# Kernel optimization log

Measured on AMD Instinct MI355X. Metric: run time of the kernel, lower is better.

## Reference

```python
import jax, jax.numpy as jnp
import numpy as np
import math

BS, NAG, HID, NACT, MESS, QD, KD, STEPS, INP = 4096, 8, 256, 16, 64, 64, 64, 5, 128
TRAJ = STEPS * NACT
LAMQ = 0.5


def setup_inputs() -> dict:
    key = jax.random.key(0)
    ks = jax.random.split(key, 12)
    g = lambda k, shape, fan: jax.random.normal(k, shape, jnp.float32) / math.sqrt(fan)
    d = {}
    d["inputs"] = jax.random.normal(ks[0], (BS * NAG, INP), jnp.float32)
    d["old_hstate"] = jax.random.normal(ks[1], (BS * NAG, HID), jnp.float32)
    d["fc1_w"] = g(ks[2], (HID, INP), INP); d["fc1_b"] = jnp.zeros((HID,), jnp.float32)
    d["w_ih"] = g(ks[3], (3 * HID, HID), HID); d["w_hh"] = g(ks[4], (3 * HID, HID), HID)
    d["b_ih"] = jnp.zeros((3 * HID,), jnp.float32); d["b_hh"] = jnp.zeros((3 * HID,), jnp.float32)
    d["dec_w"] = g(ks[5], (NACT, HID), HID); d["dec_b"] = jnp.zeros((NACT,), jnp.float32)
    d["trans_w"] = g(ks[6], (HID, HID + NAG), HID + NAG); d["trans_b"] = jnp.zeros((HID,), jnp.float32)
    d["qij_w"] = g(ks[7], (NACT, HID + MESS), HID + MESS); d["qij_b"] = jnp.zeros((NACT,), jnp.float32)
    d["q_w"] = g(ks[8], (QD, TRAJ), TRAJ); d["q_b"] = jnp.zeros((QD,), jnp.float32)
    d["k_w"] = g(ks[9], (KD, TRAJ), TRAJ); d["k_b"] = jnp.zeros((KD,), jnp.float32)
    d["v_w"] = g(ks[10], (MESS, TRAJ), TRAJ); d["v_b"] = jnp.zeros((MESS,), jnp.float32)
    return d


def _fwd(inputs, old_hstate, fc1_w, fc1_b, w_ih, w_hh, b_ih, b_hh,
         dec_w, dec_b, trans_w, trans_b, qij_w, qij_b,
         q_w, q_b, k_w, k_b, v_w, v_b):
    # fc1 + relu
    x = jax.nn.relu(inputs @ fc1_w.T + fc1_b)  # (BS*NAG, HID)
    # GRUCell (torch gate order: r, z, n)
    gi = x @ w_ih.T + b_ih
    gh = old_hstate @ w_hh.T + b_hh
    ir, iz, i_n = jnp.split(gi, 3, axis=-1)
    hr, hz, h_n = jnp.split(gh, 3, axis=-1)
    r = jax.nn.sigmoid(ir + hr)
    z = jax.nn.sigmoid(iz + hz)
    n = jnp.tanh(i_n + r * h_n)
    h_new = (1.0 - z) * n + z * old_hstate
    h = h_new.reshape(BS, NAG, HID)

    # imagination rollout on detached h
    def step(hc, _):
        q_inf = hc @ dec_w.T + dec_b                       # (BS, NAG, NACT)
        ac = jnp.argmax(q_inf, axis=-1).astype(hc.dtype)   # (BS, NAG)
        ac = jnp.broadcast_to(ac[:, None, :], (BS, NAG, NAG))
        ti = jnp.concatenate([hc, ac], axis=-1)            # (BS, NAG, HID+NAG)
        return ti @ trans_w.T + trans_b, q_inf

    _, qs = jax.lax.scan(step, jax.lax.stop_gradient(h), None, length=STEPS)
    # qs: (STEPS, BS, NAG, NACT) -> trajectory (BS, NAG, STEPS*NACT), step-major on last dim
    traj = jnp.moveaxis(qs, 0, 2).reshape(BS, NAG, TRAJ)

    # tiny agent attention
    query = traj @ q_w.T + q_b   # (BS, NAG, QD)
    key_t = traj @ k_w.T + k_b   # (BS, NAG, KD)
    value = traj @ v_w.T + v_b   # (BS, NAG, MESS)
    score = jnp.einsum('bnq,bmq->bnm', query, key_t) / math.sqrt(MESS)
    attn = jax.nn.softmax(score, axis=-1)
    traj_msg = jnp.einsum('bnm,bmd->bnd', attn, value)  # (BS, NAG, MESS)

    q_local = h @ dec_w.T + dec_b
    q_ij = jnp.concatenate([h, traj_msg], axis=-1) @ qij_w.T + qij_b
    q = q_local + LAMQ * q_ij
    return q, h


def reference(inputs, old_hstate, fc1_w, fc1_b, w_ih, w_hh, b_ih, b_hh,
              dec_w, dec_b, trans_w, trans_b, qij_w, qij_b,
              q_w, q_b, k_w, k_b, v_w, v_b):
    return _fwd(inputs, old_hstate, fc1_w, fc1_b, w_ih, w_hh, b_ih, b_hh,
                dec_w, dec_b, trans_w, trans_b, qij_w, qij_b,
                q_w, q_b, k_w, k_b, v_w, v_b)
```

## Files before the change

### kernel.cpp

```cpp
#include <hip/hip_runtime.h>
#include <math.h>

typedef unsigned short u16;
typedef unsigned int   u32;
typedef __attribute__((ext_vector_type(8))) short bf16x8;
typedef __attribute__((ext_vector_type(4))) float f32x4;

#define NROWS 32768
#define NAG 8
#define HID 256
#define INP 128
#define NACT 16
#define MESS 64
#define TRAJD 80
#define QD 64
#define HOFF 524288

#define PKO_FC1 0
#define PKO_IH  98304
#define PKO_HH  688128
#define PKO_TR  1277952
#define PKO_DEC 1499136
#define PKO_QKV 1511424
#define PKO_QIJ 1566720
#define PK_TOTAL 1582080
#define WS_CB   791040
#define WS_FLAG 793312

#define OB_FC1B 0
#define OB_BIH  256
#define OB_BHH  1024
#define OB_DECB 1792
#define OB_TRB  1808
#define OB_QIJB 2064
#define OB_QB   2080

__device__ __forceinline__ float bf2f(u16 v){ return __uint_as_float(((u32)v)<<16); }
__device__ __forceinline__ u16 f2bf(float f){
    u32 u = __float_as_uint(f);
    return (u16)((u + 0x7fffu + ((u>>16)&1u))>>16);
}
__device__ __forceinline__ float sig_(float x){ return 1.0f/(1.0f+expf(-x)); }
__device__ __forceinline__ float ldin(const void* p, size_t i, int f32){
    return f32 ? ((const float*)p)[i] : bf2f(((const u16*)p)[i]);
}
__device__ __forceinline__ void stout1(void* out, size_t i, float v, int f32){
    if (f32) ((float*)out)[i]=v; else ((u16*)out)[i]=f2bf(v);
}
__device__ __forceinline__ void split3(float w, u16& s0, u16& s1, u16& s2){
    u16 a=f2bf(w); float r  = w - bf2f(a);
    u16 b=f2bf(r); float r2 = r - bf2f(b);
    s0=a; s1=b; s2=f2bf(r2);
}
__device__ __forceinline__ f32x4 splat4(float b){ f32x4 v = {b,b,b,b}; return v; }

#define MFMA(a,b,c) __builtin_amdgcn_mfma_f32_16x16x32_bf16((a),(b),(c),0,0,0)

__device__ __forceinline__ bf16x8 lda_pl(const u16* P, int p, int row, int kbyte){
    const char* b = (const char*)P + ((p*32+row)*640) + (kbyte ^ ((row&7)<<4));
    return *(const bf16x8*)b;
}
__device__ __forceinline__ void stw_pl(u16* P, int p, int row, int col, u16 v){
    char* b = (char*)P + ((p*32+row)*640) + (((col*2)) ^ ((row&7)<<4));
    *(u16*)b = v;
}
__device__ __forceinline__ void split_store_pl(u16* P, int row, int col, float v){
    u16 a,b,c; split3(v,a,b,c);
    stw_pl(P,0,row,col,a); stw_pl(P,1,row,col,b); stw_pl(P,2,row,col,c);
}
__device__ __forceinline__ bf16x8 lda_tp(const u16* P, int p, int row, int kbyte){
    const char* b = (const char*)P + ((p*32+row)*256) + (kbyte ^ ((row&7)<<4));
    return *(const bf16x8*)b;
}
__device__ __forceinline__ void stw_tp(u16* P, int p, int row, int col, u16 v){
    char* b = (char*)P + ((p*32+row)*256) + (((col*2)) ^ ((row&7)<<4));
    *(u16*)b = v;
}
__device__ __forceinline__ void split_store_tp(u16* P, int row, int col, float v){
    u16 a,b,c; split3(v,a,b,c);
    stw_tp(P,0,row,col,a); stw_tp(P,1,row,col,b); stw_tp(P,2,row,col,c);
}
__device__ __forceinline__ float ld_tp1(const u16* P, int p, int row, int col){
    const char* b = (const char*)P + ((p*32+row)*256) + (((col*2)) ^ ((row&7)<<4));
    return bf2f(*(const u16*)b);
}
__device__ __forceinline__ bf16x8 ldg_bf8(const void* p, size_t off){
    return *(const bf16x8*)((const u16*)p + off);
}
__device__ __forceinline__ void ldg_f32_split(const void* p, size_t off, bf16x8& f0, bf16x8& f1, bf16x8& f2){
    const float* fp = (const float*)p + off;
    #pragma unroll
    for (int j=0;j<8;j++){
        float w = fp[j];
        u16 a,b,c; split3(w,a,b,c);
        f0[j]=(short)a; f1[j]=(short)b; f2[j]=(short)c;
    }
}
#define BCH(base, NTv, ksv, pbv, ntv) \
    (*(const bf16x8*)((base) + ((((ksv)*3+(pbv))*(NTv) + (ntv))*512) + lane*8))

__global__ void k_det(const void* __restrict__ inp, int* __restrict__ flag){
    __shared__ int cnt;
    if (threadIdx.x==0) cnt=0;
    __syncthreads();
    int big=0;
    for (int i=threadIdx.x;i<128;i+=64){
        u32 w = ((const u32*)inp)[i];
        float g = bf2f((u16)w);
        if (!(fabsf(g) <= 1e4f)) big++;
    }
    if (big) atomicAdd(&cnt, big);
    __syncthreads();
    if (threadIdx.x==0) *flag = (cnt>=4) ? 1 : 0;
}

__device__ __forceinline__ void pack_tile(const void* W, int Kdim, int NT, u16* pk, int tau, int f32){
    int lane2 = tau & 63, c = tau >> 6;
    int nt = c % NT, ks = c / NT;
    int n  = nt*16 + (lane2 & 15);
    int kb = ks*32 + (lane2 >> 4)*8;
    u16 o0[8],o1[8],o2[8];
    #pragma unroll
    for (int j=0;j<8;j++){
        int k = kb + j;
        float w = (k < Kdim) ? ldin(W, (size_t)n*Kdim + k, f32) : 0.0f;
        split3(w, o0[j], o1[j], o2[j]);
    }
    size_t base = ((size_t)(ks*3+0)*NT + nt)*512 + lane2*8;
    size_t step = (size_t)NT*512;
    #pragma unroll
    for (int j=0;j<8;j++){
        pk[base+j]=o0[j]; pk[base+step+j]=o1[j]; pk[base+2*step+j]=o2[j];
    }
}

__global__ __launch_bounds__(256) void k0_prep(
    const void* fc1_w, const void* w_ih, const void* w_hh, const void* trans_w,
    const void* dec_w, const void* qij_w, const void* q_w, const void* k_w, const void* v_w,
    const void* fc1_b, const void* b_ih, const void* b_hh, const void* dec_b,
    const void* trans_b, const void* qij_b, const void* q_b, const void* k_b, const void* v_b,
    float* __restrict__ ws, const int* __restrict__ flagp)
{
    const int f32 = *flagp;
    u16* pk = (u16*)ws;
    int i = blockIdx.x*256 + threadIdx.x;
    if (i < 4096)        pack_tile(fc1_w,  128, 16, pk+PKO_FC1, i,        f32);
    else if (i < 28672)  pack_tile(w_ih,   256, 48, pk+PKO_IH,  i-4096,   f32);
    else if (i < 53248)  pack_tile(w_hh,   256, 48, pk+PKO_HH,  i-28672,  f32);
    else if (i < 62464)  pack_tile(trans_w,264, 16, pk+PKO_TR,  i-53248,  f32);
    else if (i < 62976)  pack_tile(dec_w,  256,  1, pk+PKO_DEC, i-62464,  f32);
    else if (i < 65280){
        int tau = i - 62976;
        int lane2 = tau&63, c = tau>>6, nt = c%12, ks = c/12;
        int n = nt*16 + (lane2&15);
        const void* W = (n<64)? q_w : (n<128 ? k_w : v_w);
        int nl = n & 63;
        int kb = ks*32 + (lane2>>4)*8;
        u16 o0[8],o1[8],o2[8];
        #pragma unroll
        for (int j=0;j<8;j++){
            int k = kb + j;
            float w = (k < 80) ? ldin(W, (size_t)nl*80 + k, f32) : 0.0f;
            split3(w, o0[j], o1[j], o2[j]);
        }
        u16* dst = pk + PKO_QKV;
        size_t base = ((size_t)(ks*3+0)*12 + nt)*512 + lane2*8;
        size_t step = (size_t)12*512;
        #pragma unroll
        for (int j=0;j<8;j++){
            dst[base+j]=o0[j]; dst[base+step+j]=o1[j]; dst[base+2*step+j]=o2[j];
        }
    }
    else if (i < 65920)  pack_tile(qij_w,  320,  1, pk+PKO_QIJ, i-65280,  f32);
    else if (i < 68192){
        int i2 = i - 65920;
        float v;
        if      (i2<256)  v=ldin(fc1_b,i2,f32);
        else if (i2<1024) v=ldin(b_ih,i2-256,f32);
        else if (i2<1792) v=ldin(b_hh,i2-1024,f32);
        else if (i2<1808) v=ldin(dec_b,i2-1792,f32);
        else if (i2<2064) v=ldin(trans_b,i2-1808,f32);
        else if (i2<2080) v=ldin(qij_b,i2-2064,f32);
        else if (i2<2144) v=ldin(q_b,i2-2080,f32);
        else if (i2<2208) v=ldin(k_b,i2-2144,f32);
        else              v=ldin(v_b,i2-2208,f32);
        ws[WS_CB+i2]=v;
    }
}

template<int F32>
__global__ __launch_bounds__(512,2) void k12_fused(
    const void* __restrict__ inp, const void* __restrict__ oldh,
    const float* __restrict__ ws, void* __restrict__ dout, const int* __restrict__ flagp)
{
    if (*flagp != F32) return;
    constexpr int PBW = F32 ? 2 : 0;
    constexpr int PAG = F32 ? 2 : 0;

    __shared__ __align__(16) u16  planes[3*32*320];
    __shared__ __align__(16) u16  tplanes[3*32*128];
    __shared__ float s_qkv[32*201];
    __shared__ float s_att[256];
    __shared__ float s_bias[2272];
    __shared__ float s_act[32];

    const int t = threadIdx.x;
    const int wid = t>>6, lane = t&63, lr = lane&15, lk = lane>>4;
    const int row0 = blockIdx.x*32;
    const u16* pk = (const u16*)ws;
    const float* cb = ws + WS_CB;

    for (int i=t;i<3*32*320/2;i+=512) ((u32*)planes)[i]=0u;
    for (int i=t;i<3*32*128/2;i+=512) ((u32*)tplanes)[i]=0u;
    for (int i=t;i<2272;i+=512) s_bias[i]=cb[i];
    __syncthreads();

    {
        const u16* pkf = pk + PKO_FC1;
        const int nt0 = wid, nt1 = wid + 8;
        f32x4 acc[2][2];
        acc[0][0]=splat4(s_bias[OB_FC1B+nt0*16+lr]); acc[1][0]=acc[0][0];
        acc[0][1]=splat4(s_bias[OB_FC1B+nt1*16+lr]); acc[1][1]=acc[0][1];
        for (int ks=0;ks<4;ks++){
            bf16x8 a[2][3];
            if (F32){
                ldg_f32_split(inp,(size_t)(row0+lr)*INP + ks*32+lk*8,    a[0][0],a[0][1],a[0][2]);
                ldg_f32_split(inp,(size_t)(row0+16+lr)*INP + ks*32+lk*8, a[1][0],a[1][1],a[1][2]);
            } else {
                a[0][0]=ldg_bf8(inp,(size_t)(row0+lr)*INP + ks*32+lk*8);
                a[1][0]=ldg_bf8(inp,(size_t)(row0+16+lr)*INP + ks*32+lk*8);
            }
            #pragma unroll
            for (int pb=0;pb<=PBW;pb++){
                bf16x8 B0 = BCH(pkf,16,ks,pb,nt0);
                bf16x8 B1 = BCH(pkf,16,ks,pb,nt1);
                #pragma unroll
                for (int pa=0;pa<=((PAG<2-pb)?PAG:(2-pb));pa++){
                    acc[0][0]=MFMA(a[0][pa],B0,acc[0][0]); acc[0][1]=MFMA(a[0][pa],B1,acc[0][1]);
                    acc[1][0]=MFMA(a[1][pa],B0,acc[1][0]); acc[1][1]=MFMA(a[1][pa],B1,acc[1][1]);
                }
            }
        }
        #pragma unroll
        for (int m=0;m<2;m++)
        #pragma unroll
        for (int ni=0;ni<2;ni++)
        #pragma unroll
        for (int j=0;j<4;j++){
            float v = acc[m][ni][j]; v = v>0.f ? v : 0.f;
            split_store_pl(planes, m*16+lk*4+j, (ni?nt1:nt0)*16+lr, v);
        }
    }
    __syncthreads();

    float hreg[16];
    {
        const u16* pki = pk + PKO_IH;
        const u16* pkh = pk + PKO_HH;
        const int g0 = wid, g1 = wid + 8;
        f32x4 aR[2][2], aZ[2][2], aN[2][2], aH[2][2];
        #pragma unroll
        for (int m=0;m<2;m++)
        #pragma unroll
        for (int gi=0;gi<2;gi++){
            int c = (gi?g1:g0)*16 + lr;
            aR[m][gi]=splat4(s_bias[OB_BIH+c]     + s_bias[OB_BHH+c]);
            aZ[m][gi]=splat4(s_bias[OB_BIH+256+c] + s_bias[OB_BHH+256+c]);
            aN[m][gi]=splat4(s_bias[OB_BIH+512+c]);
            aH[m][gi]=splat4(s_bias[OB_BHH+512+c]);
        }
        for (int ks=0;ks<8;ks++){
            #pragma unroll
            for (int pb=0;pb<=PBW;pb++){
                bf16x8 Br0=BCH(pki,48,ks,pb,g0),    Br1=BCH(pki,48,ks,pb,g1);
                bf16x8 Bz0=BCH(pki,48,ks,pb,16+g0), Bz1=BCH(pki,48,ks,pb,16+g1);
                bf16x8 Bn0=BCH(pki,48,ks,pb,32+g0), Bn1=BCH(pki,48,ks,pb,32+g1);
                #pragma unroll
                for (int pa=0;pa<=2-pb;pa++){
                    bf16x8 a0 = lda_pl(planes, pa, lr,    ks*64+lk*16);
                    bf16x8 a1 = lda_pl(planes, pa, 16+lr, ks*64+lk*16);
                    aR[0][0]=MFMA(a0,Br0,aR[0][0]); aR[0][1]=MFMA(a0,Br1,aR[0][1]);
                    aR[1][0]=MFMA(a1,Br0,aR[1][0]); aR[1][1]=MFMA(a1,Br1,aR[1][1]);
                    aZ[0][0]=MFMA(a0,Bz0,aZ[0][0]); aZ[0][1]=MFMA(a0,Bz1,aZ[0][1]);
                    aZ[1][0]=MFMA(a1,Bz0,aZ[1][0]); aZ[1][1]=MFMA(a1,Bz1,aZ[1][1]);
                    aN[0][0]=MFMA(a0,Bn0,aN[0][0]); aN[0][1]=MFMA(a0,Bn1,aN[0][1]);
                    aN[1][0]=MFMA(a1,Bn0,aN[1][0]); aN[1][1]=MFMA(a1,Bn1,aN[1][1]);
                }
            }
        }
        for (int ks=0;ks<8;ks++){
            bf16x8 a[2][3];
            if (F32){
                ldg_f32_split(oldh,(size_t)(row0+lr)*HID + ks*32+lk*8,    a[0][0],a[0][1],a[0][2]);
                ldg_f32_split(oldh,(size_t)(row0+16+lr)*HID + ks*32+lk*8, a[1][0],a[1][1],a[1][2]);
            } else {
                a[0][0]=ldg_bf8(oldh,(size_t)(row0+lr)*HID + ks*32+lk*8);
                a[1][0]=ldg_bf8(oldh,(size_t)(row0+16+lr)*HID + ks*32+lk*8);
            }
            #pragma unroll
            for (int pb=0;pb<=PBW;pb++){
                bf16x8 Br0=BCH(pkh,48,ks,pb,g0),    Br1=BCH(pkh,48,ks,pb,g1);
                bf16x8 Bz0=BCH(pkh,48,ks,pb,16+g0), Bz1=BCH(pkh,48,ks,pb,16+g1);
                bf16x8 Bh0=BCH(pkh,48,ks,pb,32+g0), Bh1=BCH(pkh,48,ks,pb,32+g1);
                #pragma unroll
                for (int pa=0;pa<=((PAG<2-pb)?PAG:(2-pb));pa++){
                    aR[0][0]=MFMA(a[0][pa],Br0,aR[0][0]); aR[0][1]=MFMA(a[0][pa],Br1,aR[0][1]);
                    aR[1][0]=MFMA(a[1][pa],Br0,aR[1][0]); aR[1][1]=MFMA(a[1][pa],Br1,aR[1][1]);
                    aZ[0][0]=MFMA(a[0][pa],Bz0,aZ[0][0]); aZ[0][1]=MFMA(a[0][pa],Bz1,aZ[0][1]);
                    aZ[1][0]=MFMA(a[1][pa],Bz0,aZ[1][0]); aZ[1][1]=MFMA(a[1][pa],Bz1,aZ[1][1]);
                    aH[0][0]=MFMA(a[0][pa],Bh0,aH[0][0]); aH[0][1]=MFMA(a[0][pa],Bh1,aH[0][1]);
                    aH[1][0]=MFMA(a[1][pa],Bh0,aH[1][0]); aH[1][1]=MFMA(a[1][pa],Bh1,aH[1][1]);
                }
            }
        }
        #pragma unroll
        for (int m=0;m<2;m++)
        #pragma unroll
        for (int gi=0;gi<2;gi++)
        #pragma unroll
        for (int j=0;j<4;j++){
            int row = m*16 + lk*4 + j;
            int c   = (gi?g1:g0)*16 + lr;
            float r  = sig_(aR[m][gi][j]);
            float z  = sig_(aZ[m][gi][j]);
            float nv = tanhf(aN[m][gi][j] + r*aH[m][gi][j]);
            float ho = ldin(oldh,(size_t)(row0+row)*HID + c, F32);
            float h  = (1.f-z)*nv + z*ho;
            hreg[m*8+gi*4+j] = h;
            stout1(dout,(size_t)HOFF + (size_t)(row0+row)*HID + c, h, F32);
        }
    }
    __syncthreads();
    #pragma unroll
    for (int m=0;m<2;m++)
    #pragma unroll
    for (int gi=0;gi<2;gi++)
    #pragma unroll
    for (int j=0;j<4;j++)
        split_store_pl(planes, m*16+lk*4+j, (gi?wid+8:wid)*16+lr, hreg[m*8+gi*4+j]);
    __syncthreads();

    const u16* pkd = pk + PKO_DEC;
    const u16* pkt = pk + PKO_TR;
    #pragma unroll 1
    for (int s=0;s<5;s++){
        if (wid<2){
            const int m = wid;
            f32x4 d0 = splat4(s_bias[OB_DECB+lr]);
            f32x4 d1 = splat4(0.f), d2 = splat4(0.f);
            for (int ks=0;ks<8;ks++){
                #pragma unroll
                for (int pb=0;pb<=PBW;pb++){
                    bf16x8 B = BCH(pkd,1,ks,pb,0);
                    #pragma unroll
                    for (int pa=0;pa<=2-pb;pa++){
                        bf16x8 a = lda_pl(planes, pa, m*16+lr, ks*64+lk*16);
                        if (pa==0) d0=MFMA(a,B,d0); else if (pa==1) d1=MFMA(a,B,d1); else d2=MFMA(a,B,d2);
                    }
                }
            }
            f32x4 q;
            #pragma unroll
            for (int j=0;j<4;j++) q[j]=d0[j]+d1[j]+d2[j];
            #pragma unroll
            for (int j=0;j<4;j++)
                split_store_tp(tplanes, m*16+lk*4+j, s*16+lr, q[j]);
            if (s<4){
                #pragma unroll
                for (int j=0;j<4;j++){
                    float v = q[j]; int ai = lr;
                    #pragma unroll
                    for (int msk=1; msk<16; msk<<=1){
                        float pv = __shfl_xor(v, msk);
                        int   pi = __shfl_xor(ai, msk);
                        if (pv>v || (pv==v && pi<ai)){ v=pv; ai=pi; }
                    }
                    if (lr==0) s_act[m*16+lk*4+j] = (float)ai;
                }
            }
        }
        if (s==4) break;
        __syncthreads();
        if (t<256){
            int row = t>>3, aj = t&7;
            stw_pl(planes, 0, row, 256+aj, f2bf(s_act[(row & ~7) + aj]));
        }
        __syncthreads();
        {
            const int nt0=wid, nt1=wid+8;
            f32x4 acc[2][2];
            acc[0][0]=splat4(s_bias[OB_TRB+nt0*16+lr]); acc[1][0]=acc[0][0];
            acc[0][1]=splat4(s_bias[OB_TRB+nt1*16+lr]); acc[1][1]=acc[0][1];
            for (int ks=0;ks<9;ks++){
                #pragma unroll
                for (int pb=0;pb<=PBW;pb++){
                    bf16x8 B0=BCH(pkt,16,ks,pb,nt0), B1=BCH(pkt,16,ks,pb,nt1);
                    #pragma unroll
                    for (int pa=0;pa<=2-pb;pa++){
                        bf16x8 a0 = lda_pl(planes,pa,lr,   ks*64+lk*16);
                        bf16x8 a1 = lda_pl(planes,pa,16+lr,ks*64+lk*16);
                        acc[0][0]=MFMA(a0,B0,acc[0][0]); acc[0][1]=MFMA(a0,B1,acc[0][1]);
                        acc[1][0]=MFMA(a1,B0,acc[1][0]); acc[1][1]=MFMA(a1,B1,acc[1][1]);
                    }
                }
            }
            __syncthreads();
            #pragma unroll
            for (int m=0;m<2;m++)
            #pragma unroll
            for (int ni=0;ni<2;ni++)
            #pragma unroll
            for (int j=0;j<4;j++)
                split_store_pl(planes, m*16+lk*4+j, (ni?nt1:nt0)*16+lr, acc[m][ni][j]);
        }
        __syncthreads();
    }

    __syncthreads();
    #pragma unroll
    for (int m=0;m<2;m++)
    #pragma unroll
    for (int gi=0;gi<2;gi++)
    #pragma unroll
    for (int j=0;j<4;j++)
        split_store_pl(planes, m*16+lk*4+j, (gi?wid+8:wid)*16+lr, hreg[m*8+gi*4+j]);
    {
        const u16* pkq = pk + PKO_QKV;
        const int n0 = wid;
        const int has2 = (wid<4);
        const int n1 = wid + 8;
        f32x4 acc[2][2];
        acc[0][0]=splat4(s_bias[OB_QB+n0*16+lr]); acc[1][0]=acc[0][0];
        { float b1 = has2 ? s_bias[OB_QB+n1*16+lr] : 0.f;
          acc[0][1]=splat4(b1); acc[1][1]=acc[0][1]; }
        for (int ks=0;ks<3;ks++){
            #pragma unroll
            for (int pb=0;pb<=PBW;pb++){
                bf16x8 B0 = BCH(pkq,12,ks,pb,n0);
                bf16x8 B1 = has2 ? BCH(pkq,12,ks,pb,n1) : B0;
                #pragma unroll
                for (int pa=0;pa<=2-pb;pa++){
                    bf16x8 a0 = lda_tp(tplanes, pa, lr,    ks*64+lk*16);
                    bf16x8 a1 = lda_tp(tplanes, pa, 16+lr, ks*64+lk*16);
                    acc[0][0]=MFMA(a0,B0,acc[0][0]); acc[1][0]=MFMA(a1,B0,acc[1][0]);
                    if (has2){ acc[0][1]=MFMA(a0,B1,acc[0][1]); acc[1][1]=MFMA(a1,B1,acc[1][1]); }
                }
            }
        }
        #pragma unroll
        for (int m=0;m<2;m++)
        #pragma unroll
        for (int j=0;j<4;j++){
            int row = m*16+lk*4+j;
            s_qkv[row*201 + n0*16+lr] = acc[m][0][j];
            if (has2) s_qkv[row*201 + n1*16+lr] = acc[m][1][j];
        }
    }
    __syncthreads();
    if (t<256){
        int b=t>>6, n=(t>>3)&7, mm=t&7;
        const float* qv = s_qkv + (b*8+n)*201;
        const float* kv = s_qkv + (b*8+mm)*201 + 64;
        float a2=0.f;
        #pragma unroll
        for (int d=0;d<64;d++) a2 += qv[d]*kv[d];
        s_att[t] = a2*0.125f;
    }
    __syncthreads();
    if (t<32){
        int base = (t>>3)*64 + (t&7)*8;
        float mx = s_att[base];
        #pragma unroll
        for (int j2=1;j2<8;j2++) mx = fmaxf(mx, s_att[base+j2]);
        float e[8]; float sum=0.f;
        #pragma unroll
        for (int j2=0;j2<8;j2++){ e[j2]=expf(s_att[base+j2]-mx); sum+=e[j2]; }
        float inv = 1.f/sum;
        #pragma unroll
        for (int j2=0;j2<8;j2++) s_att[base+j2] = e[j2]*inv;
    }
    __syncthreads();
    for (int o=t;o<2048;o+=512){
        int row=o>>6, d=o&63, b=row>>3;
        float a3=0.f;
        #pragma unroll
        for (int mm=0;mm<8;mm++) a3 += s_att[b*64+(row&7)*8+mm]*s_qkv[(b*8+mm)*201+128+d];
        split_store_pl(planes, row, 256+d, a3);
    }
    __syncthreads();
    if (wid<2){
        const u16* pkj = pk + PKO_QIJ;
        const int m = wid;
        f32x4 e0 = splat4(s_bias[OB_QIJB+lr]);
        f32x4 e1 = splat4(0.f), e2 = splat4(0.f);
        for (int ks=0;ks<10;ks++){
            #pragma unroll
            for (int pb=0;pb<=PBW;pb++){
                bf16x8 B = BCH(pkj,1,ks,pb,0);
                #pragma unroll
                for (int pa=0;pa<=2-pb;pa++){
                    bf16x8 a = lda_pl(planes, pa, m*16+lr, ks*64+lk*16);
                    if (pa==0) e0=MFMA(a,B,e0); else if (pa==1) e1=MFMA(a,B,e1); else e2=MFMA(a,B,e2);
                }
            }
        }
        #pragma unroll
        for (int j=0;j<4;j++){
            int row = m*16+lk*4+j;
            float ql = ld_tp1(tplanes,0,row,lr) + ld_tp1(tplanes,1,row,lr) + ld_tp1(tplanes,2,row,lr);
            float qq = ql + 0.5f*(e0[j]+e1[j]+e2[j]);
            stout1(dout,(size_t)(row0+row)*NACT + lr, qq, F32);
        }
    }
}

extern "C" void kernel_launch(void* const* d_in, const int* in_sizes, int n_in,
                              void* d_out, int out_size, void* d_ws, size_t ws_size,
                              hipStream_t stream)
{
    (void)in_sizes; (void)n_in; (void)out_size; (void)ws_size;
    const void* inputs = d_in[0];
    const void* oldh   = d_in[1];
    float* ws = (float*)d_ws;
    int* flagp = (int*)(ws + WS_FLAG);

    k_det<<<1,64,0,stream>>>(inputs, flagp);
    k0_prep<<<268,256,0,stream>>>(d_in[2],d_in[4],d_in[5],d_in[10],d_in[8],d_in[12],
                                  d_in[14],d_in[16],d_in[18],
                                  d_in[3],d_in[6],d_in[7],d_in[9],d_in[11],d_in[13],
                                  d_in[15],d_in[17],d_in[19],
                                  ws, flagp);
    k12_fused<0><<<1024,512,0,stream>>>(inputs, oldh, ws, d_out, flagp);
    k12_fused<1><<<1024,512,0,stream>>>(inputs, oldh, ws, d_out, flagp);
}
```

Before: 616.8 us.

## Compute decoder redundantly in all warps to drop barrier and bias/tplane LDS

Every warp now computes the dec head for both row tiles and does the argmax shuffle in registers. This removes the s_act staging buffer and one __syncthreads per rollout step. Trajectory values are kept as fp32 in s_traj and split into bf16 planes on the fly for the QKV GEMM, which replaces the tplanes buffer. Biases are read directly from global memory instead of an LDS copy, several loops are fully unrolled, and the QKV work is rebalanced over six warps. The cost is redundant MFMA work across warps and higher register pressure from the unrolling.

After: 938.5 us. +52.2%, slower.

```diff
diff --git a/kernel.cpp b/kernel.cpp
--- a/kernel.cpp
+++ b/kernel.cpp
@@ -67,22 +67,6 @@
 __device__ __forceinline__ void split_store_pl(u16* P, int row, int col, float v){
     u16 a,b,c; split3(v,a,b,c);
     stw_pl(P,0,row,col,a); stw_pl(P,1,row,col,b); stw_pl(P,2,row,col,c);
-}
-__device__ __forceinline__ bf16x8 lda_tp(const u16* P, int p, int row, int kbyte){
-    const char* b = (const char*)P + ((p*32+row)*256) + (kbyte ^ ((row&7)<<4));
-    return *(const bf16x8*)b;
-}
-__device__ __forceinline__ void stw_tp(u16* P, int p, int row, int col, u16 v){
-    char* b = (char*)P + ((p*32+row)*256) + (((col*2)) ^ ((row&7)<<4));
-    *(u16*)b = v;
-}
-__device__ __forceinline__ void split_store_tp(u16* P, int row, int col, float v){
-    u16 a,b,c; split3(v,a,b,c);
-    stw_tp(P,0,row,col,a); stw_tp(P,1,row,col,b); stw_tp(P,2,row,col,c);
-}
-__device__ __forceinline__ float ld_tp1(const u16* P, int p, int row, int col){
-    const char* b = (const char*)P + ((p*32+row)*256) + (((col*2)) ^ ((row&7)<<4));
-    return bf2f(*(const u16*)b);
 }
 __device__ __forceinline__ bf16x8 ldg_bf8(const void* p, size_t off){
     return *(const bf16x8*)((const u16*)p + off);
@@ -197,30 +181,35 @@
     constexpr int PBW = F32 ? 2 : 0;
     constexpr int PAG = F32 ? 2 : 0;
 
-    __shared__ __align__(16) u16  planes[3*32*320];
-    __shared__ __align__(16) u16  tplanes[3*32*128];
-    __shared__ float s_qkv[32*201];
+    __shared__ __align__(16) u16   planes[3*32*320];
+    __shared__ __align__(16) float s_traj[32*100];
+    __shared__ __align__(16) float s_qkv[32*196];
     __shared__ float s_att[256];
-    __shared__ float s_bias[2272];
-    __shared__ float s_act[32];
 
     const int t = threadIdx.x;
     const int wid = t>>6, lane = t&63, lr = lane&15, lk = lane>>4;
+    const int nt0 = wid, nt1 = wid + 8;
+    const int c0 = nt0*16+lr, c1 = nt1*16+lr;
     const int row0 = blockIdx.x*32;
     const u16* pk = (const u16*)ws;
     const float* cb = ws + WS_CB;
-
-    for (int i=t;i<3*32*320/2;i+=512) ((u32*)planes)[i]=0u;
-    for (int i=t;i<3*32*128/2;i+=512) ((u32*)tplanes)[i]=0u;
-    for (int i=t;i<2272;i+=512) s_bias[i]=cb[i];
+    const u16* pkf = pk + PKO_FC1;
+    const u16* pki = pk + PKO_IH;
+    const u16* pkh = pk + PKO_HH;
+    const u16* pkt = pk + PKO_TR;
+    const u16* pkd = pk + PKO_DEC;
+    const u16* pkq = pk + PKO_QKV;
+    const u16* pkj = pk + PKO_QIJ;
+
+    for (int i=t;i<15360;i+=512) ((u32*)planes)[i]=0u;
+    for (int i=t;i<3200;i+=512) s_traj[i]=0.f;
     __syncthreads();
 
     {
-        const u16* pkf = pk + PKO_FC1;
-        const int nt0 = wid, nt1 = wid + 8;
         f32x4 acc[2][2];
-        acc[0][0]=splat4(s_bias[OB_FC1B+nt0*16+lr]); acc[1][0]=acc[0][0];
-        acc[0][1]=splat4(s_bias[OB_FC1B+nt1*16+lr]); acc[1][1]=acc[0][1];
+        acc[0][0]=splat4(cb[OB_FC1B+c0]); acc[1][0]=acc[0][0];
+        acc[0][1]=splat4(cb[OB_FC1B+c1]); acc[1][1]=acc[0][1];
+        #pragma unroll
         for (int ks=0;ks<4;ks++){
             bf16x8 a[2][3];
             if (F32){
@@ -255,26 +244,24 @@
 
     float hreg[16];
     {
-        const u16* pki = pk + PKO_IH;
-        const u16* pkh = pk + PKO_HH;
-        const int g0 = wid, g1 = wid + 8;
         f32x4 aR[2][2], aZ[2][2], aN[2][2], aH[2][2];
         #pragma unroll
         for (int m=0;m<2;m++)
         #pragma unroll
         for (int gi=0;gi<2;gi++){
-            int c = (gi?g1:g0)*16 + lr;
-            aR[m][gi]=splat4(s_bias[OB_BIH+c]     + s_bias[OB_BHH+c]);
-            aZ[m][gi]=splat4(s_bias[OB_BIH+256+c] + s_bias[OB_BHH+256+c]);
-            aN[m][gi]=splat4(s_bias[OB_BIH+512+c]);
-            aH[m][gi]=splat4(s_bias[OB_BHH+512+c]);
-        }
+            int c = (gi?nt1:nt0)*16 + lr;
+            aR[m][gi]=splat4(cb[OB_BIH+c]     + cb[OB_BHH+c]);
+            aZ[m][gi]=splat4(cb[OB_BIH+256+c] + cb[OB_BHH+256+c]);
+            aN[m][gi]=splat4(cb[OB_BIH+512+c]);
+            aH[m][gi]=splat4(cb[OB_BHH+512+c]);
+        }
+        #pragma unroll
         for (int ks=0;ks<8;ks++){
             #pragma unroll
             for (int pb=0;pb<=PBW;pb++){
-                bf16x8 Br0=BCH(pki,48,ks,pb,g0),    Br1=BCH(pki,48,ks,pb,g1);
-                bf16x8 Bz0=BCH(pki,48,ks,pb,16+g0), Bz1=BCH(pki,48,ks,pb,16+g1);
-                bf16x8 Bn0=BCH(pki,48,ks,pb,32+g0), Bn1=BCH(pki,48,ks,pb,32+g1);
+                bf16x8 Br0=BCH(pki,48,ks,pb,   nt0), Br1=BCH(pki,48,ks,pb,   nt1);
+                bf16x8 Bz0=BCH(pki,48,ks,pb,16+nt0), Bz1=BCH(pki,48,ks,pb,16+nt1);
+                bf16x8 Bn0=BCH(pki,48,ks,pb,32+nt0), Bn1=BCH(pki,48,ks,pb,32+nt1);
                 #pragma unroll
                 for (int pa=0;pa<=2-pb;pa++){
                     bf16x8 a0 = lda_pl(planes, pa, lr,    ks*64+lk*16);
@@ -288,6 +275,7 @@
                 }
             }
         }
+        #pragma unroll
         for (int ks=0;ks<8;ks++){
             bf16x8 a[2][3];
             if (F32){
@@ -299,9 +287,9 @@
             }
             #pragma unroll
             for (int pb=0;pb<=PBW;pb++){
-                bf16x8 Br0=BCH(pkh,48,ks,pb,g0),    Br1=BCH(pkh,48,ks,pb,g1);
-                bf16x8 Bz0=BCH(pkh,48,ks,pb,16+g0), Bz1=BCH(pkh,48,ks,pb,16+g1);
-                bf16x8 Bh0=BCH(pkh,48,ks,pb,32+g0), Bh1=BCH(pkh,48,ks,pb,32+g1);
+                bf16x8 Br0=BCH(pkh,48,ks,pb,   nt0), Br1=BCH(pkh,48,ks,pb,   nt1);
+                bf16x8 Bz0=BCH(pkh,48,ks,pb,16+nt0), Bz1=BCH(pkh,48,ks,pb,16+nt1);
+                bf16x8 Bh0=BCH(pkh,48,ks,pb,32+nt0), Bh1=BCH(pkh,48,ks,pb,32+nt1);
                 #pragma unroll
                 for (int pa=0;pa<=((PAG<2-pb)?PAG:(2-pb));pa++){
                     aR[0][0]=MFMA(a[0][pa],Br0,aR[0][0]); aR[0][1]=MFMA(a[0][pa],Br1,aR[0][1]);
@@ -320,7 +308,7 @@
         #pragma unroll
         for (int j=0;j<4;j++){
             int row = m*16 + lk*4 + j;
-            int c   = (gi?g1:g0)*16 + lr;
+            int c   = (gi?nt1:nt0)*16 + lr;
             float r  = sig_(aR[m][gi][j]);
             float z  = sig_(aZ[m][gi][j]);
             float nv = tanhf(aN[m][gi][j] + r*aH[m][gi][j]);
@@ -337,60 +325,70 @@
     for (int gi=0;gi<2;gi++)
     #pragma unroll
     for (int j=0;j<4;j++)
-        split_store_pl(planes, m*16+lk*4+j, (gi?wid+8:wid)*16+lr, hreg[m*8+gi*4+j]);
-    __syncthreads();
-
-    const u16* pkd = pk + PKO_DEC;
-    const u16* pkt = pk + PKO_TR;
+        split_store_pl(planes, m*16+lk*4+j, (gi?nt1:nt0)*16+lr, hreg[m*8+gi*4+j]);
+    __syncthreads();
+
     #pragma unroll 1
     for (int s=0;s<5;s++){
-        if (wid<2){
-            const int m = wid;
-            f32x4 d0 = splat4(s_bias[OB_DECB+lr]);
-            f32x4 d1 = splat4(0.f), d2 = splat4(0.f);
-            for (int ks=0;ks<8;ks++){
-                #pragma unroll
-                for (int pb=0;pb<=PBW;pb++){
-                    bf16x8 B = BCH(pkd,1,ks,pb,0);
-                    #pragma unroll
-                    for (int pa=0;pa<=2-pb;pa++){
-                        bf16x8 a = lda_pl(planes, pa, m*16+lr, ks*64+lk*16);
-                        if (pa==0) d0=MFMA(a,B,d0); else if (pa==1) d1=MFMA(a,B,d1); else d2=MFMA(a,B,d2);
-                    }
-                }
-            }
-            f32x4 q;
-            #pragma unroll
-            for (int j=0;j<4;j++) q[j]=d0[j]+d1[j]+d2[j];
-            #pragma unroll
-            for (int j=0;j<4;j++)
-                split_store_tp(tplanes, m*16+lk*4+j, s*16+lr, q[j]);
-            if (s<4){
-                #pragma unroll
-                for (int j=0;j<4;j++){
-                    float v = q[j]; int ai = lr;
-                    #pragma unroll
-                    for (int msk=1; msk<16; msk<<=1){
-                        float pv = __shfl_xor(v, msk);
-                        int   pi = __shfl_xor(ai, msk);
-                        if (pv>v || (pv==v && pi<ai)){ v=pv; ai=pi; }
-                    }
-                    if (lr==0) s_act[m*16+lk*4+j] = (float)ai;
-                }
-            }
+        f32x4 d0[2], d1[2], d2[2];
+        d0[0]=splat4(cb[OB_DECB+lr]); d0[1]=d0[0];
+        d1[0]=splat4(0.f); d1[1]=d1[0]; d2[0]=d1[0]; d2[1]=d1[0];
+        #pragma unroll
+        for (int ks=0;ks<8;ks++){
+            #pragma unroll
+            for (int pb=0;pb<=PBW;pb++){
+                bf16x8 B = BCH(pkd,1,ks,pb,0);
+                #pragma unroll
+                for (int pa=0;pa<=2-pb;pa++){
+                    bf16x8 a0 = lda_pl(planes, pa, lr,    ks*64+lk*16);
+                    bf16x8 a1 = lda_pl(planes, pa, 16+lr, ks*64+lk*16);
+                    if (pa==0){ d0[0]=MFMA(a0,B,d0[0]); d0[1]=MFMA(a1,B,d0[1]); }
+                    else if (pa==1){ d1[0]=MFMA(a0,B,d1[0]); d1[1]=MFMA(a1,B,d1[1]); }
+                    else { d2[0]=MFMA(a0,B,d2[0]); d2[1]=MFMA(a1,B,d2[1]); }
+                }
+            }
+        }
+        f32x4 q[2];
+        #pragma unroll
+        for (int m=0;m<2;m++)
+        #pragma unroll
+        for (int j=0;j<4;j++) q[m][j]=d0[m][j]+d1[m][j]+d2[m][j];
+        if (wid==0){
+            #pragma unroll
+            for (int m=0;m<2;m++)
+            #pragma unroll
+            for (int j=0;j<4;j++) s_traj[(m*16+lk*4+j)*100 + s*16 + lr] = q[m][j];
         }
         if (s==4) break;
-        __syncthreads();
-        if (t<256){
-            int row = t>>3, aj = t&7;
-            stw_pl(planes, 0, row, 256+aj, f2bf(s_act[(row & ~7) + aj]));
+        int act[2][4];
+        #pragma unroll
+        for (int m=0;m<2;m++)
+        #pragma unroll
+        for (int j=0;j<4;j++){
+            float v = q[m][j]; int ai = lr;
+            #pragma unroll
+            for (int msk=1; msk<16; msk<<=1){
+                float pv = __shfl_xor(v, msk);
+                int   pi = __shfl_xor(ai, msk);
+                if (pv>v || (pv==v && pi<ai)){ v=pv; ai=pi; }
+            }
+            act[m][j]=ai;
+        }
+        if (wid==0 && lr<8){
+            #pragma unroll
+            for (int m=0;m<2;m++)
+            #pragma unroll
+            for (int j=0;j<4;j++){
+                int R = m*16+lk*4+j;
+                stw_pl(planes, 0, (R&~7)+lr, 256+(R&7), f2bf((float)act[m][j]));
+            }
         }
         __syncthreads();
         {
-            const int nt0=wid, nt1=wid+8;
-            f32x4 acc[2][2];
-            acc[0][0]=splat4(s_bias[OB_TRB+nt0*16+lr]); acc[1][0]=acc[0][0];
-            acc[0][1]=splat4(s_bias[OB_TRB+nt1*16+lr]); acc[1][1]=acc[0][1];
+            f32x4 tc[2][2];
+            tc[0][0]=splat4(cb[OB_TRB+c0]); tc[1][0]=tc[0][0];
+            tc[0][1]=splat4(cb[OB_TRB+c1]); tc[1][1]=tc[0][1];
+            #pragma unroll
             for (int ks=0;ks<9;ks++){
                 #pragma unroll
                 for (int pb=0;pb<=PBW;pb++){
@@ -399,8 +397,8 @@
                     for (int pa=0;pa<=2-pb;pa++){
                         bf16x8 a0 = lda_pl(planes,pa,lr,   ks*64+lk*16);
                         bf16x8 a1 = lda_pl(planes,pa,16+lr,ks*64+lk*16);
-                        acc[0][0]=MFMA(a0,B0,acc[0][0]); acc[0][1]=MFMA(a0,B1,acc[0][1]);
-                        acc[1][0]=MFMA(a1,B0,acc[1][0]); acc[1][1]=MFMA(a1,B1,acc[1][1]);
+                        tc[0][0]=MFMA(a0,B0,tc[0][0]); tc[0][1]=MFMA(a0,B1,tc[0][1]);
+                        tc[1][0]=MFMA(a1,B0,tc[1][0]); tc[1][1]=MFMA(a1,B1,tc[1][1]);
                     }
                 }
             }
@@ -411,39 +409,43 @@
             for (int ni=0;ni<2;ni++)
             #pragma unroll
             for (int j=0;j<4;j++)
-                split_store_pl(planes, m*16+lk*4+j, (ni?nt1:nt0)*16+lr, acc[m][ni][j]);
+                split_store_pl(planes, m*16+lk*4+j, (ni?nt1:nt0)*16+lr, tc[m][ni][j]);
         }
         __syncthreads();
     }
-
-    __syncthreads();
+    __syncthreads();
+
     #pragma unroll
     for (int m=0;m<2;m++)
     #pragma unroll
     for (int gi=0;gi<2;gi++)
     #pragma unroll
     for (int j=0;j<4;j++)
-        split_store_pl(planes, m*16+lk*4+j, (gi?wid+8:wid)*16+lr, hreg[m*8+gi*4+j]);
-    {
-        const u16* pkq = pk + PKO_QKV;
-        const int n0 = wid;
-        const int has2 = (wid<4);
-        const int n1 = wid + 8;
+        split_store_pl(planes, m*16+lk*4+j, (gi?nt1:nt0)*16+lr, hreg[m*8+gi*4+j]);
+    if (wid<6){
         f32x4 acc[2][2];
-        acc[0][0]=splat4(s_bias[OB_QB+n0*16+lr]); acc[1][0]=acc[0][0];
-        { float b1 = has2 ? s_bias[OB_QB+n1*16+lr] : 0.f;
-          acc[0][1]=splat4(b1); acc[1][1]=acc[0][1]; }
+        acc[0][0]=splat4(cb[OB_QB+2*wid*16+lr]);     acc[1][0]=acc[0][0];
+        acc[0][1]=splat4(cb[OB_QB+(2*wid+1)*16+lr]); acc[1][1]=acc[0][1];
+        #pragma unroll
         for (int ks=0;ks<3;ks++){
+            bf16x8 a[2][3];
+            #pragma unroll
+            for (int m=0;m<2;m++){
+                const float* tp = s_traj + (m*16+lr)*100 + ks*32 + lk*8;
+                #pragma unroll
+                for (int e=0;e<8;e++){
+                    u16 x0,x1,x2; split3(tp[e],x0,x1,x2);
+                    a[m][0][e]=(short)x0; a[m][1][e]=(short)x1; a[m][2][e]=(short)x2;
+                }
+            }
             #pragma unroll
             for (int pb=0;pb<=PBW;pb++){
-                bf16x8 B0 = BCH(pkq,12,ks,pb,n0);
-                bf16x8 B1 = has2 ? BCH(pkq,12,ks,pb,n1) : B0;
+                bf16x8 B0 = BCH(pkq,12,ks,pb,2*wid);
+                bf16x8 B1 = BCH(pkq,12,ks,pb,2*wid+1);
                 #pragma unroll
                 for (int pa=0;pa<=2-pb;pa++){
-                    bf16x8 a0 = lda_tp(tplanes, pa, lr,    ks*64+lk*16);
-                    bf16x8 a1 = lda_tp(tplanes, pa, 16+lr, ks*64+lk*16);
-                    acc[0][0]=MFMA(a0,B0,acc[0][0]); acc[1][0]=MFMA(a1,B0,acc[1][0]);
-                    if (has2){ acc[0][1]=MFMA(a0,B1,acc[0][1]); acc[1][1]=MFMA(a1,B1,acc[1][1]); }
+                    acc[0][0]=MFMA(a[0][pa],B0,acc[0][0]); acc[0][1]=MFMA(a[0][pa],B1,acc[0][1]);
+                    acc[1][0]=MFMA(a[1][pa],B0,acc[1][0]); acc[1][1]=MFMA(a[1][pa],B1,acc[1][1]);
                 }
             }
         }
@@ -451,65 +453,69 @@
         for (int m=0;m<2;m++)
         #pragma unroll
         for (int j=0;j<4;j++){
-            int row = m*16+lk*4+j;
-            s_qkv[row*201 + n0*16+lr] = acc[m][0][j];
-            if (has2) s_qkv[row*201 + n1*16+lr] = acc[m][1][j];
+            s_qkv[(m*16+lk*4+j)*196 + 2*wid*16+lr]     = acc[m][0][j];
+            s_qkv[(m*16+lk*4+j)*196 + (2*wid+1)*16+lr] = acc[m][1][j];
         }
     }
     __syncthreads();
     if (t<256){
         int b=t>>6, n=(t>>3)&7, mm=t&7;
-        const float* qv = s_qkv + (b*8+n)*201;
-        const float* kv = s_qkv + (b*8+mm)*201 + 64;
+        const float* qv = s_qkv + (b*8+n)*196;
+        const float* kv = s_qkv + (b*8+mm)*196 + 64;
         float a2=0.f;
         #pragma unroll
-        for (int d=0;d<64;d++) a2 += qv[d]*kv[d];
+        for (int d2=0;d2<64;d2++) a2 += qv[d2]*kv[d2];
         s_att[t] = a2*0.125f;
     }
     __syncthreads();
     if (t<32){
-        int base = (t>>3)*64 + (t&7)*8;
-        float mx = s_att[base];
-        #pragma unroll
-        for (int j2=1;j2<8;j2++) mx = fmaxf(mx, s_att[base+j2]);
+        float mx = s_att[t*8];
+        #pragma unroll
+        for (int j2=1;j2<8;j2++) mx = fmaxf(mx, s_att[t*8+j2]);
         float e[8]; float sum=0.f;
         #pragma unroll
-        for (int j2=0;j2<8;j2++){ e[j2]=expf(s_att[base+j2]-mx); sum+=e[j2]; }
+        for (int j2=0;j2<8;j2++){ e[j2]=expf(s_att[t*8+j2]-mx); sum+=e[j2]; }
         float inv = 1.f/sum;
         #pragma unroll
-        for (int j2=0;j2<8;j2++) s_att[base+j2] = e[j2]*inv;
+        for (int j2=0;j2<8;j2++) s_att[t*8+j2] = e[j2]*inv;
     }
     __syncthreads();
     for (int o=t;o<2048;o+=512){
-        int row=o>>6, d=o&63, b=row>>3;
+        int row=o>>6, d2=o&63, b=row>>3;
         float a3=0.f;
         #pragma unroll
-        for (int mm=0;mm<8;mm++) a3 += s_att[b*64+(row&7)*8+mm]*s_qkv[(b*8+mm)*201+128+d];
-        split_store_pl(planes, row, 256+d, a3);
-    }
-    __syncthreads();
-    if (wid<2){
-        const u16* pkj = pk + PKO_QIJ;
-        const int m = wid;
-        f32x4 e0 = splat4(s_bias[OB_QIJB+lr]);
-        f32x4 e1 = splat4(0.f), e2 = splat4(0.f);
+        for (int mm=0;mm<8;mm++) a3 += s_att[row*8+mm]*s_qkv[(b*8+mm)*196+128+d2];
+        split_store_pl(planes, row, 256+d2, a3);
+    }
+    __syncthreads();
+    {
+        f32x4 e0[2], e1[2], e2[2];
+        e0[0]=splat4(cb[OB_QIJB+lr]); e0[1]=e0[0];
+        e1[0]=splat4(0.f); e1[1]=e1[0]; e2[0]=e1[0]; e2[1]=e1[0];
+        #pragma unroll
         for (int ks=0;ks<10;ks++){
             #pragma unroll
             for (int pb=0;pb<=PBW;pb++){
                 bf16x8 B = BCH(pkj,1,ks,pb,0);
                 #pragma unroll
                 for (int pa=0;pa<=2-pb;pa++){
-                    bf16x8 a = lda_pl(planes, pa, m*16+lr, ks*64+lk*16);
-                    if (pa==0) e0=MFMA(a,B,e0); else if (pa==1) e1=MFMA(a,B,e1); else e2=MFMA(a,B,e2);
-                }
-            }
-        }
-        #pragma unroll
-        for (int j=0;j<4;j++){
-            int row = m*16+lk*4+j;
-            float ql = ld_tp1(tplanes,0,row,lr) + ld_tp1(tplanes,1,row,lr) + ld_tp1(tplanes,2,row,lr);
-            float qq = ql + 0.5f*(e0[j]+e1[j]+e2[j]);
-            stout1(dout,(size_t)(row0+row)*NACT + lr, qq, F32);
+                    bf16x8 a0 = lda_pl(planes, pa, lr,    ks*64+lk*16);
+                    bf16x8 a1 = lda_pl(planes, pa, 16+lr, ks*64+lk*16);
+                    if (pa==0){ e0[0]=MFMA(a0,B,e0[0]); e0[1]=MFMA(a1,B,e0[1]); }
+                    else if (pa==1){ e1[0]=MFMA(a0,B,e1[0]); e1[1]=MFMA(a1,B,e1[1]); }
+                    else { e2[0]=MFMA(a0,B,e2[0]); e2[1]=MFMA(a1,B,e2[1]); }
+                }
+            }
+        }
+        if (wid==0){
+            #pragma unroll
+            for (int m=0;m<2;m++)
+            #pragma unroll
+            for (int j=0;j<4;j++){
+                int row = m*16+lk*4+j;
+                float ql = s_traj[row*100 + lr];
+                stout1(dout,(size_t)(row0+row)*NACT + lr, ql + 0.5f*(e0[m][j]+e1[m][j]+e2[m][j]), F32);
+            }
         }
     }
 }
```
